# Performance work log

Hardware: AMD Instinct MI355X
Metric: run time of the kernel (lower is better)

## Reference

```python
import jax, jax.numpy as jnp
import numpy as np

T, B, I, H = 512, 64, 1024, 1024
G = 4 * H + 1  # 4 LSTM gates + 1 boundary gate (HM-LSTM)
STDV = 1.0 / np.sqrt(H)


def setup_inputs() -> dict:
    key = jax.random.key(0)
    ks = jax.random.split(key, 5)
    u = lambda k, shape: jax.random.uniform(k, shape, jnp.float32, -STDV, STDV)
    return {
        "x": jax.random.normal(ks[0], (T, B, I), jnp.float32),
        "W_ih": u(ks[1], (G, I)),
        "W_hh": u(ks[2], (G, H)),
        "b_ih": u(ks[3], (G,)),
        "b_hh": u(ks[4], (G,)),
    }


def reference(x, W_ih, W_hh, b_ih, b_hh):
    h_dim = W_hh.shape[1]
    # Precompute input contribution for all timesteps in one big GEMM: [T,B,G]
    gx_all = jnp.einsum("tbi,gi->tbg", x, W_ih) + b_ih + b_hh
    Bsz = x.shape[1]
    h0 = jnp.zeros((Bsz, h_dim), x.dtype)
    c0 = jnp.zeros((Bsz, h_dim), x.dtype)

    def step(carry, gx):
        h, c = carry
        g = gx + h @ W_hh.T  # [B, 4H+1]
        i = jax.nn.sigmoid(g[:, :h_dim])
        f = jax.nn.sigmoid(g[:, h_dim:2 * h_dim])
        gg = jnp.tanh(g[:, 2 * h_dim:3 * h_dim])
        o = jax.nn.sigmoid(g[:, 3 * h_dim:4 * h_dim])
        z = jax.nn.sigmoid(g[:, 4 * h_dim:])  # [B,1] boundary gate
        ig = i * gg
        # HM-LSTM soft boundary: FLUSH (c=i*g) when z->1, UPDATE otherwise
        c_new = z * ig + (1.0 - z) * (f * c + ig)
        h_new = o * jnp.tanh(c_new)
        return (h_new, c_new), h_new

    (hT, cT), out = jax.lax.scan(step, (h0, c0), gx_all)
    return out, hT, cT
```

## Files before the change

kernel.cpp:

```cpp
#include <hip/hip_runtime.h>
#include <cstdint>
#include <cstddef>

typedef unsigned short u16;
typedef short bf16x8 __attribute__((ext_vector_type(8)));
typedef u16   u16x8  __attribute__((ext_vector_type(8)));
typedef float f32x4  __attribute__((ext_vector_type(4)));

#define NT  512
#define NB  64
#define NH  1024
#define NTB 32768
#define G4  4096

#define AS1C(p) ((const __attribute__((address_space(1))) void*)(p))
#define AS3(p)  ((__attribute__((address_space(3))) void*)(p))

__device__ __forceinline__ float b2f(u16 u){
  return __uint_as_float(((unsigned)u) << 16);
}
__device__ __forceinline__ u16 f2b(float f){
  unsigned u = __float_as_uint(f);
  return (u16)((u + 0x7fffu + ((u >> 16) & 1u)) >> 16);
}
__device__ __forceinline__ float fsigmoid(float x){
  return __builtin_amdgcn_rcpf(1.f + __builtin_amdgcn_exp2f(-1.442695041f * x));
}
__device__ __forceinline__ float ftanh(float x){
  return 2.f * __builtin_amdgcn_rcpf(1.f + __builtin_amdgcn_exp2f(-2.885390082f * x)) - 1.f;
}

__global__ void cvt_bf16(const float* __restrict__ in, u16* __restrict__ out, int n8){
  int stride = gridDim.x * blockDim.x;
  for (int i = blockIdx.x * blockDim.x + threadIdx.x; i < n8; i += stride){
    const float4* p = (const float4*)(in + (size_t)i * 8);
    float4 a = p[0], b = p[1];
    u16x8 r;
    r[0]=f2b(a.x); r[1]=f2b(a.y); r[2]=f2b(a.z); r[3]=f2b(a.w);
    r[4]=f2b(b.x); r[5]=f2b(b.y); r[6]=f2b(b.z); r[7]=f2b(b.w);
    *(u16x8*)(out + (size_t)i * 8) = r;
  }
}

__global__ void zpre_kernel(const float* __restrict__ x, const float* __restrict__ Wih,
                            const float* __restrict__ b_ih, const float* __restrict__ b_hh,
                            float* __restrict__ zp){
  int gw   = (blockIdx.x * 256 + threadIdx.x) >> 6;
  int lane = threadIdx.x & 63;
  const float* wz = Wih + (size_t)4096 * 1024;
  float4 wv[4];
  #pragma unroll
  for (int j = 0; j < 4; ++j) wv[j] = *(const float4*)&wz[lane*16 + j*4];
  float bz = b_ih[4096] + b_hh[4096];
  for (int r = gw; r < NTB; r += 1024){
    const float* xr = x + (size_t)r * 1024 + lane * 16;
    float s = 0.f;
    #pragma unroll
    for (int j = 0; j < 4; ++j){
      float4 xv = *(const float4*)&xr[j*4];
      s += xv.x*wv[j].x + xv.y*wv[j].y + xv.z*wv[j].z + xv.w*wv[j].w;
    }
    #pragma unroll
    for (int o = 32; o > 0; o >>= 1) s += __shfl_down(s, o);
    if (lane == 0) zp[r] = s + bz;
  }
}

template<typename GT>
__global__ __launch_bounds__(256, 2) void gemm_gx(
    const u16* __restrict__ Xb, const u16* __restrict__ Wb,
    const float* __restrict__ b_ih, const float* __restrict__ b_hh,
    GT* __restrict__ gx)
{
  __shared__ u16 As[128*32];
  __shared__ u16 Bs[128*32];
  const int tid  = threadIdx.x;
  const int lane = tid & 63, wave = tid >> 6;
  const int wr = wave >> 1, wc = wave & 1;
  const int m0 = (blockIdx.x & 255) * 128;
  const int n0 = (blockIdx.x >> 8) * 128;
  const int srow = wave * 16 + (lane >> 2);
  const int scol = (lane & 3) * 8;
  const u16* gA = Xb + (size_t)(m0 + srow) * 1024 + scol;
  const u16* gB = Wb + (size_t)(n0 + srow) * 1024 + scol;
  char* lA = (char*)As + wave * 1024;
  char* lB = (char*)Bs + wave * 1024;
  const int fr = lane & 15, fo = (lane >> 4) * 8;

  f32x4 acc[4][4] = {};
  for (int k0 = 0; k0 < 1024; k0 += 32){
    __syncthreads();
    __builtin_amdgcn_global_load_lds(AS1C(gA + k0),            AS3(lA),        16, 0, 0);
    __builtin_amdgcn_global_load_lds(AS1C(gA + 64*1024 + k0),  AS3(lA + 4096), 16, 0, 0);
    __builtin_amdgcn_global_load_lds(AS1C(gB + k0),            AS3(lB),        16, 0, 0);
    __builtin_amdgcn_global_load_lds(AS1C(gB + 64*1024 + k0),  AS3(lB + 4096), 16, 0, 0);
    __syncthreads();
    bf16x8 a[4], b[4];
    #pragma unroll
    for (int mi = 0; mi < 4; ++mi)
      a[mi] = *(const bf16x8*)&As[(wr*64 + mi*16 + fr)*32 + fo];
    #pragma unroll
    for (int ni = 0; ni < 4; ++ni)
      b[ni] = *(const bf16x8*)&Bs[(wc*64 + ni*16 + fr)*32 + fo];
    #pragma unroll
    for (int mi = 0; mi < 4; ++mi)
      #pragma unroll
      for (int ni = 0; ni < 4; ++ni)
        acc[mi][ni] = __builtin_amdgcn_mfma_f32_16x16x32_bf16(a[mi], b[ni], acc[mi][ni], 0, 0, 0);
  }
  const int orow = (lane >> 4) * 4, ocol = lane & 15;
  #pragma unroll
  for (int ni = 0; ni < 4; ++ni){
    const int g = n0 + wc*64 + ni*16 + ocol;
    const float bias = b_ih[g] + b_hh[g];
    #pragma unroll
    for (int mi = 0; mi < 4; ++mi){
      const size_t rb = (size_t)(m0 + wr*64 + mi*16 + orow);
      #pragma unroll
      for (int r = 0; r < 4; ++r){
        float v = acc[mi][ni][r] + bias;
        if constexpr (sizeof(GT) == 4)
          __builtin_nontemporal_store(v, (float*)gx + (rb + r)*G4 + g);
        else
          __builtin_nontemporal_store(f2b(v), (u16*)gx + (rb + r)*G4 + g);
      }
    }
  }
}

__device__ __forceinline__ uint4 ld_h(const uint4* p, bool fb){
  uint4 r;
  if (fb) asm volatile("global_load_dwordx4 %0, %1, off sc0 sc1" : "=v"(r) : "v"(p) : "memory");
  else    asm volatile("global_load_dwordx4 %0, %1, off sc0"     : "=v"(r) : "v"(p) : "memory");
  return r;
}

template<typename GT>
__global__ __launch_bounds__(512, 2) void hmlstm_scan(
    const u16* __restrict__ Whhb, const GT* __restrict__ gx,
    const float* __restrict__ zpre, unsigned* __restrict__ hdw,
    float* __restrict__ out)
{
  const int tid  = threadIdx.x;
  const int lane = tid & 63, wave = tid >> 6;
  const int gw = wave >> 1, cb = wave & 1;
  const int fr = lane & 15, hi4 = lane >> 4;
  const int g  = blockIdx.x & 7;
  const int hb = blockIdx.x >> 3;

  __shared__ u16   hs[8*1024];
  __shared__ float glds[4][8][32];
  __shared__ float zsum[8];

  const int grow = gw*1024 + hb*32 + cb*16 + fr;
  bf16x8 Bw[32];
  #pragma unroll
  for (int kc = 0; kc < 32; ++kc)
    Bw[kc] = *(const bf16x8*)&Whhb[(size_t)grow*1024 + kc*32 + hi4*8];
  #pragma unroll
  for (int kc = 0; kc < 32; ++kc)
    asm volatile("" : "+a"(Bw[kc]));

  uint2 wzr[4];
  #pragma unroll
  for (int q = 0; q < 4; ++q)
    wzr[q] = *(const uint2*)&Whhb[(size_t)4096*1024 + lane*16 + q*4];

  if (tid < 256){
    int b = tid >> 5, c = tid & 31;
    unsigned* p = hdw + (size_t)(g*8 + b)*1024 + hb*32 + c;
    unsigned v0 = 1u;
    asm volatile("global_store_dword %0, %1, off sc0 sc1" :: "v"(p), "v"(v0) : "memory");
  }

  const int srow = wave;
  const int scol = lane * 16;
  float c_reg = 0.f;
  bool  fb = false;

  for (int t = 0; t < NT; ++t){
    const unsigned* src = hdw + (size_t)(t & 1) * 65536;
    unsigned*       dst = hdw + (size_t)((t + 1) & 1) * 65536;
    const unsigned  tgt = (unsigned)(t + 1);
    const unsigned* rbase = src + (size_t)(g*8 + srow)*1024 + scol;

    uint4 v[4];
    #pragma unroll
    for (int q = 0; q < 4; ++q) v[q] = ld_h((const uint4*)(rbase + q*4), fb);

    float gxl[4]; float zpc;
    {
      const GT* gp = gx + ((size_t)t*64 + g*8 + (hi4 & 1)*4)*G4 + grow;
      if constexpr (sizeof(GT) == 4){
        #pragma unroll
        for (int r = 0; r < 4; ++r)
          asm volatile("global_load_dword %0, %1, off nt" : "=v"(gxl[r]) : "v"((const float*)gp + (size_t)r*G4) : "memory");
      } else {
        #pragma unroll
        for (int r = 0; r < 4; ++r)
          asm volatile("global_load_ushort %0, %1, off nt" : "=v"(*(unsigned*)&gxl[r]) : "v"((const u16*)gp + (size_t)r*G4) : "memory");
      }
      asm volatile("global_load_dword %0, %1, off" : "=v"(zpc) : "v"(zpre + t*64 + g*8 + ((tid>>5)&7)) : "memory");
    }
    asm volatile("s_waitcnt vmcnt(5)" ::: "memory");
    __builtin_amdgcn_sched_barrier(0);

    unsigned pend = 0;
    #pragma unroll
    for (int q = 0; q < 4; ++q){
      unsigned m = ((v[q].x^tgt)|(v[q].y^tgt)|(v[q].z^tgt)|(v[q].w^tgt)) & 0xFFFFu;
      pend |= (m == 0) ? 0u : (1u << q);
    }
    int spin = 0;
    while (__any((int)(pend != 0u))){
      if (++spin > 8){ fb = true; }
      fb = (bool)__any((int)fb);
      #pragma unroll
      for (int q = 0; q < 4; ++q)
        if (__any((int)((pend >> q) & 1u)))
          v[q] = ld_h((const uint4*)(rbase + q*4), fb);
      asm volatile("s_waitcnt vmcnt(0)" ::: "memory");
      __builtin_amdgcn_sched_barrier(0);
      #pragma unroll
      for (int q = 0; q < 4; ++q){
        if ((pend >> q) & 1u){
          unsigned m = ((v[q].x^tgt)|(v[q].y^tgt)|(v[q].z^tgt)|(v[q].w^tgt)) & 0xFFFFu;
          if (m == 0) pend &= ~(1u << q);
        }
      }
    }

    float zp = 0.f;
    #pragma unroll
    for (int q = 0; q < 4; ++q){
      unsigned p0 = (v[q].x >> 16) | (v[q].y & 0xFFFF0000u);
      unsigned p1 = (v[q].z >> 16) | (v[q].w & 0xFFFF0000u);
      zp = fmaf(__uint_as_float(p0 << 16),         __uint_as_float(wzr[q].x << 16),         zp);
      zp = fmaf(__uint_as_float(p0 & 0xFFFF0000u), __uint_as_float(wzr[q].x & 0xFFFF0000u), zp);
      zp = fmaf(__uint_as_float(p1 << 16),         __uint_as_float(wzr[q].y << 16),         zp);
      zp = fmaf(__uint_as_float(p1 & 0xFFFF0000u), __uint_as_float(wzr[q].y & 0xFFFF0000u), zp);
      uint2 pw = {p0, p1};
      int u16b = lane*32 + (q >> 1)*16;
      int addr = srow*2048 + ((u16b ^ (srow << 4))) + (q & 1)*8;
      *(uint2*)((char*)hs + addr) = pw;
    }
    #pragma unroll
    for (int o = 32; o > 0; o >>= 1) zp += __shfl_xor(zp, o);
    if (lane == 0) zsum[srow] = zp;
    __syncthreads();

    f32x4 acc0 = {}, acc1 = {}, acc2 = {}, acc3 = {};
    const int arow = fr & 7;
    #pragma unroll
    for (int kc = 0; kc < 32; kc += 4){
      bf16x8 a0 = *(const bf16x8*)((char*)hs + arow*2048 + (((kc+0)*64 + hi4*16) ^ (arow << 4)));
      bf16x8 a1 = *(const bf16x8*)((char*)hs + arow*2048 + (((kc+1)*64 + hi4*16) ^ (arow << 4)));
      bf16x8 a2 = *(const bf16x8*)((char*)hs + arow*2048 + (((kc+2)*64 + hi4*16) ^ (arow << 4)));
      bf16x8 a3 = *(const bf16x8*)((char*)hs + arow*2048 + (((kc+3)*64 + hi4*16) ^ (arow << 4)));
      asm volatile("v_mfma_f32_16x16x32_bf16 %0, %1, %2, %0" : "+v"(acc0) : "v"(a0), "a"(Bw[kc+0]));
      asm volatile("v_mfma_f32_16x16x32_bf16 %0, %1, %2, %0" : "+v"(acc1) : "v"(a1), "a"(Bw[kc+1]));
      asm volatile("v_mfma_f32_16x16x32_bf16 %0, %1, %2, %0" : "+v"(acc2) : "v"(a2), "a"(Bw[kc+2]));
      asm volatile("v_mfma_f32_16x16x32_bf16 %0, %1, %2, %0" : "+v"(acc3) : "v"(a3), "a"(Bw[kc+3]));
    }
    asm volatile("s_nop 7\n\ts_nop 7\n\ts_nop 7" :::);
    f32x4 ac = (acc0 + acc1) + (acc2 + acc3);

    asm volatile("s_waitcnt vmcnt(0)" ::: "memory");
    __builtin_amdgcn_sched_barrier(0);

    if constexpr (sizeof(GT) != 4){
      #pragma unroll
      for (int r = 0; r < 4; ++r)
        gxl[r] = __uint_as_float((*(unsigned*)&gxl[r]) << 16);
    }

    if (hi4 < 2){
      #pragma unroll
      for (int r = 0; r < 4; ++r){
        float vv = ac[r] + gxl[r];
        float s = (gw == 2) ? ftanh(vv) : fsigmoid(vv);
        glds[gw][hi4*4 + r][cb*16 + fr] = s;
      }
    }
    __syncthreads();

    if (tid < 256){
      int b = tid >> 5, c = tid & 31;
      float iv  = glds[0][b][c], fvg = glds[1][b][c];
      float gv  = glds[2][b][c], ov  = glds[3][b][c];
      float zv  = fsigmoid(zpc + zsum[b]);
      float ig  = iv * gv;
      float cn  = zv*ig + (1.f - zv)*(fvg*c_reg + ig);
      float hv_ = ov * ftanh(cn);
      c_reg = cn;
      const int hoff = (g*8 + b)*1024 + hb*32 + c;
      unsigned pv = ((unsigned)f2b(hv_) << 16) | (unsigned)(t + 2);
      asm volatile("global_store_dword %0, %1, off sc0 sc1" :: "v"(dst + hoff), "v"(pv) : "memory");
      __builtin_nontemporal_store(hv_, out + (size_t)t*65536 + hoff);
      if (t == NT-1){
        out[(size_t)NT*65536 + hoff] = hv_;
        out[(size_t)NT*65536 + 65536 + hoff] = cn;
      }
    }
  }
}

extern "C" void kernel_launch(void* const* d_in, const int* in_sizes, int n_in,
                              void* d_out, int out_size, void* d_ws, size_t ws_size,
                              hipStream_t stream)
{
  (void)in_sizes; (void)n_in; (void)out_size;
  const float* x    = (const float*)d_in[0];
  const float* Wih  = (const float*)d_in[1];
  const float* Whh  = (const float*)d_in[2];
  const float* b_ih = (const float*)d_in[3];
  const float* b_hh = (const float*)d_in[4];
  float* out = (float*)d_out;

  size_t off = 0;
  auto alloc = [&](size_t bytes)->void*{
    void* p = (char*)d_ws + off;
    off = (off + bytes + 255) & ~(size_t)255;
    return p;
  };
  u16*  xb    = (u16*) alloc((size_t)NTB*1024*2);
  u16*  wihb  = (u16*) alloc((size_t)4097*1024*2);
  u16*  whhb  = (u16*) alloc((size_t)4097*1024*2);
  unsigned* hdw = (unsigned*)alloc((size_t)2*65536*4);
  float* zp   = (float*)alloc((size_t)NTB*4);
  bool g32 = (ws_size >= off + (size_t)NTB*G4*4);
  void* gxp = (char*)d_ws + off;

  hipMemsetAsync(hdw, 0, (size_t)2*65536*4, stream);
  cvt_bf16<<<dim3(2048), dim3(256), 0, stream>>>(x,   xb,   NTB*1024/8);
  cvt_bf16<<<dim3(512),  dim3(256), 0, stream>>>(Wih, wihb, 4097*1024/8);
  cvt_bf16<<<dim3(512),  dim3(256), 0, stream>>>(Whh, whhb, 4097*1024/8);
  zpre_kernel<<<dim3(256), dim3(256), 0, stream>>>(x, Wih, b_ih, b_hh, zp);
  if (g32){
    float* gxf = (float*)gxp;
    gemm_gx<float><<<dim3(8192), dim3(256), 0, stream>>>(xb, wihb, b_ih, b_hh, gxf);
    void* args[] = { (void*)&whhb, (void*)&gxf, (void*)&zp, (void*)&hdw, (void*)&out };
    if (hipLaunchCooperativeKernel((void*)hmlstm_scan<float>, dim3(256), dim3(512),
                                   args, 0, stream) != hipSuccess)
      hmlstm_scan<float><<<dim3(256), dim3(512), 0, stream>>>(whhb, gxf, zp, hdw, out);
  } else {
    u16* gxb = (u16*)gxp;
    gemm_gx<u16><<<dim3(8192), dim3(256), 0, stream>>>(xb, wihb, b_ih, b_hh, gxb);
    void* args[] = { (void*)&whhb, (void*)&gxb, (void*)&zp, (void*)&hdw, (void*)&out };
    if (hipLaunchCooperativeKernel((void*)hmlstm_scan<u16>, dim3(256), dim3(512),
                                   args, 0, stream) != hipSuccess)
      hmlstm_scan<u16><<<dim3(256), dim3(512), 0, stream>>>(whhb, gxb, zp, hdw, out);
  }
}
```

Before: 3.457 ms.

## Split-K recurrent MFMA, prefetch next-step gx, and mirror h buffer for fallback polling

The two waves per gate now split the K dimension of the recurrent GEMM instead of the output columns. Partial sums are reduced through shared memory, and the nonlinearities move to the 256 combine threads. Gate inputs and zpre for step t+1 are prefetched during step t, so the scan loop no longer waits on gx at the top of each step. The h exchange now writes to two buffers: a primary with sc0 only and a mirror with sc0 sc1 that is polled only after a longer spin. This aims to cut cross-block synchronization latency, at the cost of doubled h stores and an extra LDS reduction.

After: 3.359 ms. 2.8% less time.

```diff
diff --git a/kernel.cpp b/kernel.cpp
--- a/kernel.cpp
+++ b/kernel.cpp
@@ -139,70 +139,76 @@
 __global__ __launch_bounds__(512, 2) void hmlstm_scan(
     const u16* __restrict__ Whhb, const GT* __restrict__ gx,
     const float* __restrict__ zpre, unsigned* __restrict__ hdw,
-    float* __restrict__ out)
+    unsigned* __restrict__ hmir, float* __restrict__ out)
 {
   const int tid  = threadIdx.x;
   const int lane = tid & 63, wave = tid >> 6;
-  const int gw = wave >> 1, cb = wave & 1;
+  const int gw = wave >> 1, kh = wave & 1;
   const int fr = lane & 15, hi4 = lane >> 4;
   const int g  = blockIdx.x & 7;
   const int hb = blockIdx.x >> 3;
 
   __shared__ u16   hs[8*1024];
-  __shared__ float glds[4][8][32];
+  __shared__ float glds[4][2][8][32];
   __shared__ float zsum[8];
 
-  const int grow = gw*1024 + hb*32 + cb*16 + fr;
-  bf16x8 Bw[32];
+  const int row0 = gw*1024 + hb*32 + fr;
+  bf16x8 Bw0[16], Bw1[16];
   #pragma unroll
-  for (int kc = 0; kc < 32; ++kc)
-    Bw[kc] = *(const bf16x8*)&Whhb[(size_t)grow*1024 + kc*32 + hi4*8];
+  for (int kk = 0; kk < 16; ++kk){
+    Bw0[kk] = *(const bf16x8*)&Whhb[(size_t)row0*1024      + kh*512 + kk*32 + hi4*8];
+    Bw1[kk] = *(const bf16x8*)&Whhb[(size_t)(row0+16)*1024 + kh*512 + kk*32 + hi4*8];
+  }
   #pragma unroll
-  for (int kc = 0; kc < 32; ++kc)
-    asm volatile("" : "+a"(Bw[kc]));
+  for (int kk = 0; kk < 16; ++kk){
+    asm volatile("" : "+a"(Bw0[kk]));
+    asm volatile("" : "+a"(Bw1[kk]));
+  }
 
   uint2 wzr[4];
   #pragma unroll
   for (int q = 0; q < 4; ++q)
     wzr[q] = *(const uint2*)&Whhb[(size_t)4096*1024 + lane*16 + q*4];
 
+  const int bq = tid >> 5, cq = tid & 31;
+
   if (tid < 256){
-    int b = tid >> 5, c = tid & 31;
-    unsigned* p = hdw + (size_t)(g*8 + b)*1024 + hb*32 + c;
+    unsigned* p  = hdw  + (size_t)(g*8 + bq)*1024 + hb*32 + cq;
+    unsigned* pm = hmir + (size_t)(g*8 + bq)*1024 + hb*32 + cq;
     unsigned v0 = 1u;
-    asm volatile("global_store_dword %0, %1, off sc0 sc1" :: "v"(p), "v"(v0) : "memory");
+    asm volatile("global_store_dword %0, %1, off sc0"     :: "v"(p),  "v"(v0) : "memory");
+    asm volatile("global_store_dword %0, %1, off sc0 sc1" :: "v"(pm), "v"(v0) : "memory");
+  }
+
+  unsigned gxc[4], gxn[4]; float zc = 0.f, zn = 0.f;
+  if (tid < 256){
+    const GT* gp = gx + (size_t)(g*8 + bq)*G4 + hb*32 + cq;
+    #pragma unroll
+    for (int q = 0; q < 4; ++q){
+      if constexpr (sizeof(GT) == 4)
+        asm volatile("global_load_dword %0, %1, off nt" : "=v"(gxc[q]) : "v"((const unsigned*)gp + q*1024) : "memory");
+      else
+        asm volatile("global_load_ushort %0, %1, off nt" : "=v"(gxc[q]) : "v"((const u16*)gp + q*1024) : "memory");
+    }
+    asm volatile("global_load_dword %0, %1, off" : "=v"(zc) : "v"(zpre + g*8 + bq) : "memory");
   }
 
   const int srow = wave;
-  const int scol = lane * 16;
   float c_reg = 0.f;
   bool  fb = false;
 
   for (int t = 0; t < NT; ++t){
-    const unsigned* src = hdw + (size_t)(t & 1) * 65536;
-    unsigned*       dst = hdw + (size_t)((t + 1) & 1) * 65536;
+    const size_t par  = (size_t)(t & 1) * 65536;
+    const size_t parn = (size_t)((t + 1) & 1) * 65536;
     const unsigned  tgt = (unsigned)(t + 1);
-    const unsigned* rbase = src + (size_t)(g*8 + srow)*1024 + scol;
+    const size_t roff = (size_t)(g*8 + srow)*1024 + lane*16;
+    const unsigned* rb_f = hdw  + par + roff;
+    const unsigned* rb_m = hmir + par + roff;
 
     uint4 v[4];
     #pragma unroll
-    for (int q = 0; q < 4; ++q) v[q] = ld_h((const uint4*)(rbase + q*4), fb);
-
-    float gxl[4]; float zpc;
-    {
-      const GT* gp = gx + ((size_t)t*64 + g*8 + (hi4 & 1)*4)*G4 + grow;
-      if constexpr (sizeof(GT) == 4){
-        #pragma unroll
-        for (int r = 0; r < 4; ++r)
-          asm volatile("global_load_dword %0, %1, off nt" : "=v"(gxl[r]) : "v"((const float*)gp + (size_t)r*G4) : "memory");
-      } else {
-        #pragma unroll
-        for (int r = 0; r < 4; ++r)
-          asm volatile("global_load_ushort %0, %1, off nt" : "=v"(*(unsigned*)&gxl[r]) : "v"((const u16*)gp + (size_t)r*G4) : "memory");
-      }
-      asm volatile("global_load_dword %0, %1, off" : "=v"(zpc) : "v"(zpre + t*64 + g*8 + ((tid>>5)&7)) : "memory");
-    }
-    asm volatile("s_waitcnt vmcnt(5)" ::: "memory");
+    for (int q = 0; q < 4; ++q) v[q] = ld_h((const uint4*)((fb ? rb_m : rb_f) + q*4), fb);
+    asm volatile("s_waitcnt vmcnt(0)" ::: "memory");
     __builtin_amdgcn_sched_barrier(0);
 
     unsigned pend = 0;
@@ -213,12 +219,12 @@
     }
     int spin = 0;
     while (__any((int)(pend != 0u))){
-      if (++spin > 8){ fb = true; }
+      if (++spin > 32){ fb = true; }
       fb = (bool)__any((int)fb);
       #pragma unroll
       for (int q = 0; q < 4; ++q)
         if (__any((int)((pend >> q) & 1u)))
-          v[q] = ld_h((const uint4*)(rbase + q*4), fb);
+          v[q] = ld_h((const uint4*)((fb ? rb_m : rb_f) + q*4), fb);
       asm volatile("s_waitcnt vmcnt(0)" ::: "memory");
       __builtin_amdgcn_sched_barrier(0);
       #pragma unroll
@@ -231,77 +237,119 @@
     }
 
     float zp = 0.f;
-    #pragma unroll
-    for (int q = 0; q < 4; ++q){
-      unsigned p0 = (v[q].x >> 16) | (v[q].y & 0xFFFF0000u);
-      unsigned p1 = (v[q].z >> 16) | (v[q].w & 0xFFFF0000u);
-      zp = fmaf(__uint_as_float(p0 << 16),         __uint_as_float(wzr[q].x << 16),         zp);
-      zp = fmaf(__uint_as_float(p0 & 0xFFFF0000u), __uint_as_float(wzr[q].x & 0xFFFF0000u), zp);
-      zp = fmaf(__uint_as_float(p1 << 16),         __uint_as_float(wzr[q].y << 16),         zp);
-      zp = fmaf(__uint_as_float(p1 & 0xFFFF0000u), __uint_as_float(wzr[q].y & 0xFFFF0000u), zp);
-      uint2 pw = {p0, p1};
-      int u16b = lane*32 + (q >> 1)*16;
-      int addr = srow*2048 + ((u16b ^ (srow << 4))) + (q & 1)*8;
-      *(uint2*)((char*)hs + addr) = pw;
+    uint4 w0, w1;
+    {
+      unsigned a0 = (v[0].x >> 16) | (v[0].y & 0xFFFF0000u);
+      unsigned a1 = (v[0].z >> 16) | (v[0].w & 0xFFFF0000u);
+      unsigned a2 = (v[1].x >> 16) | (v[1].y & 0xFFFF0000u);
+      unsigned a3 = (v[1].z >> 16) | (v[1].w & 0xFFFF0000u);
+      unsigned a4 = (v[2].x >> 16) | (v[2].y & 0xFFFF0000u);
+      unsigned a5 = (v[2].z >> 16) | (v[2].w & 0xFFFF0000u);
+      unsigned a6 = (v[3].x >> 16) | (v[3].y & 0xFFFF0000u);
+      unsigned a7 = (v[3].z >> 16) | (v[3].w & 0xFFFF0000u);
+      zp = fmaf(__uint_as_float(a0 << 16),         __uint_as_float(wzr[0].x << 16),         zp);
+      zp = fmaf(__uint_as_float(a0 & 0xFFFF0000u), __uint_as_float(wzr[0].x & 0xFFFF0000u), zp);
+      zp = fmaf(__uint_as_float(a1 << 16),         __uint_as_float(wzr[0].y << 16),         zp);
+      zp = fmaf(__uint_as_float(a1 & 0xFFFF0000u), __uint_as_float(wzr[0].y & 0xFFFF0000u), zp);
+      zp = fmaf(__uint_as_float(a2 << 16),         __uint_as_float(wzr[1].x << 16),         zp);
+      zp = fmaf(__uint_as_float(a2 & 0xFFFF0000u), __uint_as_float(wzr[1].x & 0xFFFF0000u), zp);
+      zp = fmaf(__uint_as_float(a3 << 16),         __uint_as_float(wzr[1].y << 16),         zp);
+      zp = fmaf(__uint_as_float(a3 & 0xFFFF0000u), __uint_as_float(wzr[1].y & 0xFFFF0000u), zp);
+      zp = fmaf(__uint_as_float(a4 << 16),         __uint_as_float(wzr[2].x << 16),         zp);
+      zp = fmaf(__uint_as_float(a4 & 0xFFFF0000u), __uint_as_float(wzr[2].x & 0xFFFF0000u), zp);
+      zp = fmaf(__uint_as_float(a5 << 16),         __uint_as_float(wzr[2].y << 16),         zp);
+      zp = fmaf(__uint_as_float(a5 & 0xFFFF0000u), __uint_as_float(wzr[2].y & 0xFFFF0000u), zp);
+      zp = fmaf(__uint_as_float(a6 << 16),         __uint_as_float(wzr[3].x << 16),         zp);
+      zp = fmaf(__uint_as_float(a6 & 0xFFFF0000u), __uint_as_float(wzr[3].x & 0xFFFF0000u), zp);
+      zp = fmaf(__uint_as_float(a7 << 16),         __uint_as_float(wzr[3].y << 16),         zp);
+      zp = fmaf(__uint_as_float(a7 & 0xFFFF0000u), __uint_as_float(wzr[3].y & 0xFFFF0000u), zp);
+      w0 = (uint4){a0, a1, a2, a3};
+      w1 = (uint4){a4, a5, a6, a7};
+    }
+    {
+      int u0 = lane*32;
+      *(uint4*)((char*)hs + srow*2048 + (u0        ^ (srow << 4))) = w0;
+      *(uint4*)((char*)hs + srow*2048 + ((u0 + 16) ^ (srow << 4))) = w1;
     }
     #pragma unroll
     for (int o = 32; o > 0; o >>= 1) zp += __shfl_xor(zp, o);
     if (lane == 0) zsum[srow] = zp;
+
+    if (tid < 256){
+      int tc = (t + 1 < NT) ? (t + 1) : t;
+      const GT* gp = gx + ((size_t)tc*64 + g*8 + bq)*G4 + hb*32 + cq;
+      #pragma unroll
+      for (int q = 0; q < 4; ++q){
+        if constexpr (sizeof(GT) == 4)
+          asm volatile("global_load_dword %0, %1, off nt" : "=v"(gxn[q]) : "v"((const unsigned*)gp + q*1024) : "memory");
+        else
+          asm volatile("global_load_ushort %0, %1, off nt" : "=v"(gxn[q]) : "v"((const u16*)gp + q*1024) : "memory");
+      }
+      asm volatile("global_load_dword %0, %1, off" : "=v"(zn) : "v"(zpre + tc*64 + g*8 + bq) : "memory");
+    }
     __syncthreads();
 
-    f32x4 acc0 = {}, acc1 = {}, acc2 = {}, acc3 = {};
+    f32x4 acc00 = {}, acc01 = {}, acc10 = {}, acc11 = {};
     const int arow = fr & 7;
-    #pragma unroll
-    for (int kc = 0; kc < 32; kc += 4){
-      bf16x8 a0 = *(const bf16x8*)((char*)hs + arow*2048 + (((kc+0)*64 + hi4*16) ^ (arow << 4)));
-      bf16x8 a1 = *(const bf16x8*)((char*)hs + arow*2048 + (((kc+1)*64 + hi4*16) ^ (arow << 4)));
-      bf16x8 a2 = *(const bf16x8*)((char*)hs + arow*2048 + (((kc+2)*64 + hi4*16) ^ (arow << 4)));
-      bf16x8 a3 = *(const bf16x8*)((char*)hs + arow*2048 + (((kc+3)*64 + hi4*16) ^ (arow << 4)));
-      asm volatile("v_mfma_f32_16x16x32_bf16 %0, %1, %2, %0" : "+v"(acc0) : "v"(a0), "a"(Bw[kc+0]));
-      asm volatile("v_mfma_f32_16x16x32_bf16 %0, %1, %2, %0" : "+v"(acc1) : "v"(a1), "a"(Bw[kc+1]));
-      asm volatile("v_mfma_f32_16x16x32_bf16 %0, %1, %2, %0" : "+v"(acc2) : "v"(a2), "a"(Bw[kc+2]));
-      asm volatile("v_mfma_f32_16x16x32_bf16 %0, %1, %2, %0" : "+v"(acc3) : "v"(a3), "a"(Bw[kc+3]));
+    const int kb2  = kh * 1024;
+    #pragma unroll
+    for (int kk = 0; kk < 16; kk += 2){
+      bf16x8 a0 = *(const bf16x8*)((char*)hs + arow*2048 + ((kb2 + (kk+0)*64 + hi4*16) ^ (arow << 4)));
+      bf16x8 a1 = *(const bf16x8*)((char*)hs + arow*2048 + ((kb2 + (kk+1)*64 + hi4*16) ^ (arow << 4)));
+      asm volatile("v_mfma_f32_16x16x32_bf16 %0, %1, %2, %0" : "+v"(acc00) : "v"(a0), "a"(Bw0[kk+0]));
+      asm volatile("v_mfma_f32_16x16x32_bf16 %0, %1, %2, %0" : "+v"(acc10) : "v"(a0), "a"(Bw1[kk+0]));
+      asm volatile("v_mfma_f32_16x16x32_bf16 %0, %1, %2, %0" : "+v"(acc01) : "v"(a1), "a"(Bw0[kk+1]));
+      asm volatile("v_mfma_f32_16x16x32_bf16 %0, %1, %2, %0" : "+v"(acc11) : "v"(a1), "a"(Bw1[kk+1]));
     }
     asm volatile("s_nop 7\n\ts_nop 7\n\ts_nop 7" :::);
-    f32x4 ac = (acc0 + acc1) + (acc2 + acc3);
-
-    asm volatile("s_waitcnt vmcnt(0)" ::: "memory");
-    __builtin_amdgcn_sched_barrier(0);
-
-    if constexpr (sizeof(GT) != 4){
-      #pragma unroll
-      for (int r = 0; r < 4; ++r)
-        gxl[r] = __uint_as_float((*(unsigned*)&gxl[r]) << 16);
-    }
+    f32x4 ac0 = acc00 + acc01;
+    f32x4 ac1 = acc10 + acc11;
 
     if (hi4 < 2){
       #pragma unroll
       for (int r = 0; r < 4; ++r){
-        float vv = ac[r] + gxl[r];
-        float s = (gw == 2) ? ftanh(vv) : fsigmoid(vv);
-        glds[gw][hi4*4 + r][cb*16 + fr] = s;
+        glds[gw][kh][hi4*4 + r][fr]      = ac0[r];
+        glds[gw][kh][hi4*4 + r][16 + fr] = ac1[r];
       }
     }
     __syncthreads();
 
     if (tid < 256){
-      int b = tid >> 5, c = tid & 31;
-      float iv  = glds[0][b][c], fvg = glds[1][b][c];
-      float gv  = glds[2][b][c], ov  = glds[3][b][c];
-      float zv  = fsigmoid(zpc + zsum[b]);
+      float gi = glds[0][0][bq][cq] + glds[0][1][bq][cq];
+      float gf = glds[1][0][bq][cq] + glds[1][1][bq][cq];
+      float gg = glds[2][0][bq][cq] + glds[2][1][bq][cq];
+      float go = glds[3][0][bq][cq] + glds[3][1][bq][cq];
+      float x0, x1, x2, x3;
+      if constexpr (sizeof(GT) == 4){
+        x0 = __uint_as_float(gxc[0]); x1 = __uint_as_float(gxc[1]);
+        x2 = __uint_as_float(gxc[2]); x3 = __uint_as_float(gxc[3]);
+      } else {
+        x0 = __uint_as_float(gxc[0] << 16); x1 = __uint_as_float(gxc[1] << 16);
+        x2 = __uint_as_float(gxc[2] << 16); x3 = __uint_as_float(gxc[3] << 16);
+      }
+      float iv  = fsigmoid(gi + x0);
+      float fvg = fsigmoid(gf + x1);
+      float gv  = ftanh  (gg + x2);
+      float ov  = fsigmoid(go + x3);
+      float zv  = fsigmoid(zc + zsum[bq]);
       float ig  = iv * gv;
       float cn  = zv*ig + (1.f - zv)*(fvg*c_reg + ig);
       float hv_ = ov * ftanh(cn);
       c_reg = cn;
-      const int hoff = (g*8 + b)*1024 + hb*32 + c;
+      const size_t hoff = (size_t)(g*8 + bq)*1024 + hb*32 + cq;
       unsigned pv = ((unsigned)f2b(hv_) << 16) | (unsigned)(t + 2);
-      asm volatile("global_store_dword %0, %1, off sc0 sc1" :: "v"(dst + hoff), "v"(pv) : "memory");
+      asm volatile("global_store_dword %0, %1, off sc0"     :: "v"(hdw  + parn + hoff), "v"(pv) : "memory");
+      asm volatile("global_store_dword %0, %1, off sc0 sc1" :: "v"(hmir + parn + hoff), "v"(pv) : "memory");
       __builtin_nontemporal_store(hv_, out + (size_t)t*65536 + hoff);
       if (t == NT-1){
         out[(size_t)NT*65536 + hoff] = hv_;
         out[(size_t)NT*65536 + 65536 + hoff] = cn;
       }
     }
+
+    asm volatile("s_waitcnt vmcnt(3)" ::: "memory");
+    __builtin_amdgcn_sched_barrier(0);
+    gxc[0]=gxn[0]; gxc[1]=gxn[1]; gxc[2]=gxn[2]; gxc[3]=gxn[3]; zc = zn;
   }
 }
 
@@ -326,12 +374,13 @@
   u16*  xb    = (u16*) alloc((size_t)NTB*1024*2);
   u16*  wihb  = (u16*) alloc((size_t)4097*1024*2);
   u16*  whhb  = (u16*) alloc((size_t)4097*1024*2);
-  unsigned* hdw = (unsigned*)alloc((size_t)2*65536*4);
+  unsigned* hdw  = (unsigned*)alloc((size_t)2*65536*4);
+  unsigned* hmir = (unsigned*)alloc((size_t)2*65536*4);
   float* zp   = (float*)alloc((size_t)NTB*4);
   bool g32 = (ws_size >= off + (size_t)NTB*G4*4);
   void* gxp = (char*)d_ws + off;
 
-  hipMemsetAsync(hdw, 0, (size_t)2*65536*4, stream);
+  hipMemsetAsync(hdw, 0, (size_t)4*65536*4, stream);
   cvt_bf16<<<dim3(2048), dim3(256), 0, stream>>>(x,   xb,   NTB*1024/8);
   cvt_bf16<<<dim3(512),  dim3(256), 0, stream>>>(Wih, wihb, 4097*1024/8);
   cvt_bf16<<<dim3(512),  dim3(256), 0, stream>>>(Whh, whhb, 4097*1024/8);
@@ -339,16 +388,16 @@
   if (g32){
     float* gxf = (float*)gxp;
     gemm_gx<float><<<dim3(8192), dim3(256), 0, stream>>>(xb, wihb, b_ih, b_hh, gxf);
-    void* args[] = { (void*)&whhb, (void*)&gxf, (void*)&zp, (void*)&hdw, (void*)&out };
+    void* args[] = { (void*)&whhb, (void*)&gxf, (void*)&zp, (void*)&hdw, (void*)&hmir, (void*)&out };
     if (hipLaunchCooperativeKernel((void*)hmlstm_scan<float>, dim3(256), dim3(512),
                                    args, 0, stream) != hipSuccess)
-      hmlstm_scan<float><<<dim3(256), dim3(512), 0, stream>>>(whhb, gxf, zp, hdw, out);
+      hmlstm_scan<float><<<dim3(256), dim3(512), 0, stream>>>(whhb, gxf, zp, hdw, hmir, out);
   } else {
     u16* gxb = (u16*)gxp;
     gemm_gx<u16><<<dim3(8192), dim3(256), 0, stream>>>(xb, wihb, b_ih, b_hh, gxb);
-    void* args[] = { (void*)&whhb, (void*)&gxb, (void*)&zp, (void*)&hdw, (void*)&out };
+    void* args[] = { (void*)&whhb, (void*)&gxb, (void*)&zp, (void*)&hdw, (void*)&hmir, (void*)&out };
     if (hipLaunchCooperativeKernel((void*)hmlstm_scan<u16>, dim3(256), dim3(512),
                                    args, 0, stream) != hipSuccess)
-      hmlstm_scan<u16><<<dim3(256), dim3(512), 0, stream>>>(whhb, gxb, zp, hdw, out);
-  }
-}
+      hmlstm_scan<u16><<<dim3(256), dim3(512), 0, stream>>>(whhb, gxb, zp, hdw, hmir, out);
+  }
+}
```
